# Performance work log

Hardware: AMD Instinct MI355X
Metric: run time of the kernel (lower is better)

Reference implementation:

```python
import jax, jax.numpy as jnp
import numpy as np
import math

B, S, D, H, DFF = 2, 2048, 1024, 16, 4096
DK = D // H
EPS = 1e-6


def setup_inputs() -> dict:
    key = jax.random.key(0)
    ks = jax.random.split(key, 12)
    s = 0.02
    return {
        "x": jax.random.normal(ks[0], (B, S, D), jnp.float32),
        "mask": jnp.ones((B, S), jnp.int32),
        "wq": jax.random.normal(ks[1], (D, D), jnp.float32) * s,
        "bq": jnp.zeros((D,), jnp.float32),
        "wk": jax.random.normal(ks[2], (D, D), jnp.float32) * s,
        "bk": jnp.zeros((D,), jnp.float32),
        "wv": jax.random.normal(ks[3], (D, D), jnp.float32) * s,
        "bv": jnp.zeros((D,), jnp.float32),
        "wo": jax.random.normal(ks[4], (D, D), jnp.float32) * s,
        "bo": jnp.zeros((D,), jnp.float32),
        "g1": jnp.ones((D,), jnp.float32),
        "b1": jnp.zeros((D,), jnp.float32),
        "g2": jnp.ones((D,), jnp.float32),
        "b2": jnp.zeros((D,), jnp.float32),
        "w1": jax.random.normal(ks[5], (DFF, D), jnp.float32) * s,
        "bf1": jnp.zeros((DFF,), jnp.float32),
        "w2": jax.random.normal(ks[6], (D, DFF), jnp.float32) * s,
        "bf2": jnp.zeros((D,), jnp.float32),
    }


def _gelu(x):
    # x * 0.5 * (1 + erf(x / sqrt(2))) -- exact erf-based GELU as in source
    return x * 0.5 * (1.0 + jax.lax.erf(x * (1.0 / math.sqrt(2.0))))


def _layernorm(x, gamma, beta):
    # torch.std uses unbiased (ddof=1); eps is OUTSIDE the sqrt in the source
    mean = jnp.mean(x, axis=-1, keepdims=True)
    std = jnp.std(x, axis=-1, keepdims=True, ddof=1)
    return gamma * (x - mean) / (std + EPS) + beta


def _block(x, mask, wq, bq, wk, bk, wv, bv, wo, bo, g1, b1, g2, b2, w1, bf1, w2, bf2):
    # multi-head attention (dropout is identity in eval mode)
    q = (x @ wq.T + bq).reshape(B, S, H, DK).transpose(0, 2, 1, 3)  # bhsd
    k = (x @ wk.T + bk).reshape(B, S, H, DK).transpose(0, 2, 1, 3)
    v = (x @ wv.T + bv).reshape(B, S, H, DK).transpose(0, 2, 1, 3)
    scores = jnp.einsum("bhsd,bhtd->bhst", q, k) / math.sqrt(DK)
    scores = jnp.where(mask[:, None, None, :] == 0, -1e9, scores)
    attn = jax.nn.softmax(scores, axis=-1)
    cv = jnp.einsum("bhst,bhtd->bhsd", attn, v)
    cv = cv.transpose(0, 2, 1, 3).reshape(B, S, D)
    hd = cv @ wo.T + bo
    # residual + norm1
    hd = _layernorm(x + hd, g1, b1)
    # position-wise FFN with erf GELU
    ff = _gelu(hd @ w1.T + bf1) @ w2.T + bf2
    return _layernorm(hd + ff, g2, b2)


def reference(x, mask, wq, bq, wk, bk, wv, bv, wo, bo, g1, b1, g2, b2, w1, bf1, w2, bf2):
    return _block(x, mask, wq, bq, wk, bk, wv, bv, wo, bo, g1, b1, g2, b2, w1, bf1, w2, bf2)
```

## Files before the change

### kernel.cpp

```cpp
#include <hip/hip_runtime.h>
#include <hip/hip_bf16.h>

#define B_   2
#define S_   2048
#define D_   1024
#define H_   16
#define DK_  64
#define DFF_ 4096
#define M_   (B_*S_)

typedef unsigned short u16;
typedef __attribute__((ext_vector_type(8))) short short8;
typedef __attribute__((ext_vector_type(4))) short bf16x4;
typedef __attribute__((ext_vector_type(4))) float floatx4;

__device__ __forceinline__ u16 f2bf(float f) {
    union { float f; unsigned u; } v; v.f = f;
    unsigned r = v.u + 0x7fffu + ((v.u >> 16) & 1u);
    return (u16)(r >> 16);
}
__device__ __forceinline__ u16 f2bf_fast(float f) {
    __hip_bfloat16 h = __float2bfloat16(f);
    return *reinterpret_cast<u16*>(&h);
}

__device__ __forceinline__ void g2l16(const u16* g, u16* l) {
    __builtin_amdgcn_global_load_lds((const __attribute__((address_space(1))) void*)g,
                                     (__attribute__((address_space(3))) void*)l,
                                     16, 0, 0);
}

__device__ __forceinline__ unsigned lds_off(const void* p) {
    return (unsigned)(unsigned long long)p;
}

#define TRB16(dst, va, IMM)                                                    \
    asm volatile("ds_read_b64_tr_b16 %0, %1 offset:" #IMM                      \
                 : "=v"(dst) : "v"(va))

__global__ __launch_bounds__(256) void cvt_all(
    const float* __restrict__ x,  const float* __restrict__ wq,
    const float* __restrict__ wk, const float* __restrict__ wv,
    const float* __restrict__ wo, const float* __restrict__ w1,
    const float* __restrict__ w2,
    u16* __restrict__ xb, u16* __restrict__ wqkvb, u16* __restrict__ wob,
    u16* __restrict__ w1b, u16* __restrict__ w2b) {
    for (int i = blockIdx.x * 256 + threadIdx.x; i < 4194304;
         i += gridDim.x * 256) {
        const float* s; u16* d; int off;
        if (i < 1048576)      { s = x;  d = xb;    off = i; }
        else if (i < 1310720) { s = wq; d = wqkvb; off = i - 1048576; }
        else if (i < 1572864) { s = wk; d = wqkvb + 1048576; off = i - 1310720; }
        else if (i < 1835008) { s = wv; d = wqkvb + 2097152; off = i - 1572864; }
        else if (i < 2097152) { s = wo; d = wob;   off = i - 1835008; }
        else if (i < 3145728) { s = w1; d = w1b;   off = i - 2097152; }
        else                  { s = w2; d = w2b;   off = i - 3145728; }
        float4 v = reinterpret_cast<const float4*>(s)[off];
        ushort4 o;
        o.x = f2bf(v.x); o.y = f2bf(v.y); o.z = f2bf(v.z); o.w = f2bf(v.w);
        reinterpret_cast<ushort4*>(d)[off] = o;
    }
}

__global__ __launch_bounds__(256) void prep_misc(const float* __restrict__ bq,
                                                 const float* __restrict__ bk,
                                                 const float* __restrict__ bv,
                                                 const int* __restrict__ mask,
                                                 float* __restrict__ bqkv,
                                                 float* __restrict__ mbias) {
    int i = blockIdx.x * 256 + threadIdx.x;
    if (i < 3 * D_) {
        float v = (i < D_) ? bq[i] : (i < 2 * D_) ? bk[i - D_] : bv[i - 2 * D_];
        bqkv[i] = v;
    } else if (i < 3 * D_ + B_ * S_) {
        int k = i - 3 * D_;
        mbias[k] = (mask[k] == 0) ? -1e9f : 0.0f;
    }
}

template <int EPI>
__global__ __launch_bounds__(512, 2) void gemm256_bt(const u16* __restrict__ A,
                                                     const u16* __restrict__ Bw,
                                                     const float* __restrict__ bias,
                                                     u16* __restrict__ Cb,
                                                     int N, int K) {
    __shared__ alignas(16) u16 sA[2][2][8192];
    __shared__ alignas(16) u16 sB[2][2][8192];
    const int tid = threadIdx.x;
    const int wid = tid >> 6, lane = tid & 63;
    const int lrow = lane & 15, lgrp = lane >> 4;
    const int wm = wid >> 2, wn = wid & 3;

    const int nbx = gridDim.x;
    const int nwg = nbx * gridDim.y;
    const int orig = blockIdx.y * nbx + blockIdx.x;
    const int qd = nwg >> 3, rr = nwg & 7, xc = orig & 7, oi = orig >> 3;
    const int swz = (xc < rr ? xc * (qd + 1) : rr * (qd + 1) + (xc - rr) * qd) + oi;
    const int m0 = (swz % nbx) * 256, n0 = (swz / nbx) * 256;

    const u16* Ab = A + (size_t)m0 * K;
    const u16* Bb = Bw + (size_t)n0 * K;
    const int T = K >> 6;

    const int c0 = (wid * 2 + 0) * 64 + lane;
    const int c1 = (wid * 2 + 1) * 64 + lane;
    const int r0 = c0 >> 3, g0 = c0 & 7;
    const int r1 = c1 >> 3, g1 = c1 & 7;
    const size_t so0 = (size_t)r0 * K + (size_t)((g0 ^ (r0 & 7)) * 8);
    const size_t so1 = (size_t)r1 * K + (size_t)((g1 ^ (r1 & 7)) * 8);
    const int d0 = (wid * 2 + 0) * 512;
    const int d1 = (wid * 2 + 1) * 512;

    auto stageA = [&](int par, int half, int kt) {
        const u16* src = Ab + (size_t)(half * 128) * K + kt * 64;
        g2l16(src + so0, &sA[par][half][d0]);
        g2l16(src + so1, &sA[par][half][d1]);
    };
    auto stageB = [&](int par, int half, int kt) {
        const u16* src = Bb + (size_t)(half * 128) * K + kt * 64;
        g2l16(src + so0, &sB[par][half][d0]);
        g2l16(src + so1, &sB[par][half][d1]);
    };

    stageA(0, 0, 0); stageA(0, 1, 0);
    stageB(0, 0, 0); stageB(0, 1, 0);
    if (T > 1) { stageB(1, 0, 1); stageB(1, 1, 1); }
    asm volatile("s_waitcnt vmcnt(4)" ::: "memory");
    asm volatile("s_barrier" ::: "memory");

    floatx4 acc[8][4] = {};
    const int rbase = (wn & 1) * 64;
    const int bhalf = wn >> 1;

    for (int t = 0; t < T; t++) {
        const int par = t & 1;
        const char* baseA = (const char*)&sA[par][wm][0];
        const char* baseB = (const char*)&sB[par][bhalf][0];
        short8 bfr[4][2];
#pragma unroll
        for (int ph = 0; ph < 4; ph++) {
            if (ph == 0) {
#pragma unroll
                for (int nj = 0; nj < 4; nj++) {
                    int rb = rbase + nj * 16 + lrow;
#pragma unroll
                    for (int kk = 0; kk < 2; kk++) {
                        int off = rb * 128 + (((kk * 4 + lgrp) ^ (lrow & 7)) * 16);
                        bfr[nj][kk] = *reinterpret_cast<const short8*>(baseB + off);
                    }
                }
            }
            short8 af[2][2];
#pragma unroll
            for (int a = 0; a < 2; a++) {
                int ra = (2 * ph + a) * 16 + lrow;
#pragma unroll
                for (int kk = 0; kk < 2; kk++) {
                    int off = ra * 128 + (((kk * 4 + lgrp) ^ (lrow & 7)) * 16);
                    af[a][kk] = *reinterpret_cast<const short8*>(baseA + off);
                }
            }
            if (ph == 0) { if (t + 1 < T) stageA(par ^ 1, 0, t + 1); }
            if (ph == 1) { if (t + 1 < T) stageA(par ^ 1, 1, t + 1); }
            if (ph == 2) { if (t + 2 < T) stageB(par, 0, t + 2); }
            if (ph == 3) { if (t + 2 < T) stageB(par, 1, t + 2); }

            asm volatile("s_barrier" ::: "memory");
            asm volatile("s_waitcnt lgkmcnt(0)" ::: "memory");
            __builtin_amdgcn_sched_barrier(0);

            __builtin_amdgcn_s_setprio(1);
#pragma unroll
            for (int a = 0; a < 2; a++)
#pragma unroll
                for (int nj = 0; nj < 4; nj++) {
                    acc[2 * ph + a][nj] = __builtin_amdgcn_mfma_f32_16x16x32_bf16(
                        af[a][0], bfr[nj][0], acc[2 * ph + a][nj], 0, 0, 0);
                    acc[2 * ph + a][nj] = __builtin_amdgcn_mfma_f32_16x16x32_bf16(
                        af[a][1], bfr[nj][1], acc[2 * ph + a][nj], 0, 0, 0);
                }
            __builtin_amdgcn_s_setprio(0);

            if (ph == 3) {
                if (t >= T - 3) asm volatile("s_waitcnt vmcnt(0)" ::: "memory");
                else            asm volatile("s_waitcnt vmcnt(4)" ::: "memory");
            }
            asm volatile("s_barrier" ::: "memory");
        }
    }

#pragma unroll
    for (int mi = 0; mi < 8; mi++) {
        int row = m0 + wm * 128 + mi * 16 + lgrp * 4;
#pragma unroll
        for (int nj = 0; nj < 4; nj++) {
            int col = n0 + wn * 64 + nj * 16 + lrow;
            float bc = bias[col];
#pragma unroll
            for (int j = 0; j < 4; j++) {
                float v = acc[mi][nj][j] + bc;
                if (EPI == 2) v = 0.5f * v * (1.0f + erff(v * 0.70710678118654752f));
                Cb[(size_t)(row + j) * N + col] = f2bf(v);
            }
        }
    }
}

template <int EPI>
__global__ __launch_bounds__(256) void gemm_bt(const u16* __restrict__ A,
                                               const u16* __restrict__ Bw,
                                               const float* __restrict__ bias,
                                               float* __restrict__ Cf,
                                               u16* __restrict__ Cb,
                                               int N, int K) {
    __shared__ u16 sA[128 * 32];
    __shared__ u16 sB[128 * 32];
    const int tid = threadIdx.x;
    const int wid = tid >> 6, lane = tid & 63;
    const int lrow = lane & 15, lgrp = lane >> 4;

    const int nbx = gridDim.x;
    const int nwg = nbx * gridDim.y;
    const int orig = blockIdx.y * nbx + blockIdx.x;
    const int qd = nwg >> 3, rr = nwg & 7, xc = orig & 7, oi = orig >> 3;
    const int swz = (xc < rr ? xc * (qd + 1) : rr * (qd + 1) + (xc - rr) * qd) + oi;
    const int m0 = (swz % nbx) * 128, n0 = (swz / nbx) * 128;

    const int wm = wid >> 1, wn = wid & 1;
    const int ar = lane >> 2, ac = lane & 3;

    floatx4 acc[4][4] = {};
    const u16* Ab = A + (size_t)m0 * K;
    const u16* Bb = Bw + (size_t)n0 * K;

    for (int k0 = 0; k0 < K; k0 += 32) {
#pragma unroll
        for (int i = 0; i < 2; i++) {
            int seg = wid * 2 + i;
            int row = seg * 16 + ar;
            g2l16(Ab + (size_t)row * K + k0 + ac * 8, &sA[seg * 512]);
            g2l16(Bb + (size_t)row * K + k0 + ac * 8, &sB[seg * 512]);
        }
        __syncthreads();
        short8 af[4], bfr[4];
#pragma unroll
        for (int mi = 0; mi < 4; mi++)
            af[mi] = *reinterpret_cast<const short8*>(
                &sA[(wm * 64 + mi * 16 + lrow) * 32 + lgrp * 8]);
#pragma unroll
        for (int ni = 0; ni < 4; ni++)
            bfr[ni] = *reinterpret_cast<const short8*>(
                &sB[(wn * 64 + ni * 16 + lrow) * 32 + lgrp * 8]);
#pragma unroll
        for (int mi = 0; mi < 4; mi++)
#pragma unroll
            for (int ni = 0; ni < 4; ni++)
                acc[mi][ni] = __builtin_amdgcn_mfma_f32_16x16x32_bf16(
                    af[mi], bfr[ni], acc[mi][ni], 0, 0, 0);
        __syncthreads();
    }

#pragma unroll
    for (int mi = 0; mi < 4; mi++) {
        int row = m0 + wm * 64 + mi * 16 + lgrp * 4;
#pragma unroll
        for (int ni = 0; ni < 4; ni++) {
            int col = n0 + wn * 64 + ni * 16 + lrow;
            float bc = bias[col];
#pragma unroll
            for (int j = 0; j < 4; j++) {
                float v = acc[mi][ni][j] + bc;
                if (EPI == 1)
                    Cf[(size_t)(row + j) * N + col] = v;
                else
                    Cb[(size_t)(row + j) * N + col] = f2bf(v);
            }
        }
    }
}

__global__ __launch_bounds__(256) void attn_kernel(const u16* __restrict__ QKV,
                                                   const float* __restrict__ mbias,
                                                   u16* __restrict__ O) {
    const int SD = 3 * D_;
    __shared__ alignas(16) u16 ktL[2][4096];
    __shared__ alignas(16) u16 vtL[2][4096];
    __shared__ alignas(16) u16 pL[4][1024];

    const int orig = blockIdx.y * gridDim.x + blockIdx.x;
    const int swz = (orig & 7) * 128 + (orig >> 3);
    const int qt = swz & 31, bh = swz >> 5;
    const int b = bh >> 4, h = bh & 15;

    const int tid = threadIdx.x, wid = tid >> 6, lane = tid & 63;
    const int lrow = lane & 15, lgrp = lane >> 4;

    const u16* Qp = QKV + h * DK_;
    const u16* Kp = QKV + D_ + h * DK_;
    const u16* Vp = QKV + 2 * D_ + h * DK_;
    const float* mbrow = mbias + b * S_;

    const int qr = qt * 64 + wid * 16 + lrow;
    const u16* qrow = Qp + (size_t)(b * S_ + qr) * SD;
    short8 aq0 = *reinterpret_cast<const short8*>(qrow + lgrp * 8);
    short8 aq1 = *reinterpret_cast<const short8*>(qrow + 32 + lgrp * 8);

    const u16* kq[2];
    const u16* vq[2];
#pragma unroll
    for (int i = 0; i < 2; i++) {
        int s = wid * 2 + i;
        int q8 = s * 64 + lane;
        int krow = q8 >> 3, kcb = q8 & 7;
        kq[i] = Kp + (size_t)(b * S_ + krow) * SD + ((kcb ^ (krow & 7)) * 8);
        int o = s * 512 + lane * 8;
        int vk = ((o >> 6) & 7) * 8 + ((o >> 9) & 1) * 4 + ((o >> 4) & 3);
        int vd = (o >> 10) * 16 + (o & 8);
        vq[i] = Vp + (size_t)(b * S_ + vk) * SD + vd;
    }

    auto issue = [&](int bufIdx) {
        u16* kb_ = ktL[bufIdx];
        u16* vb_ = vtL[bufIdx];
#pragma unroll
        for (int i = 0; i < 2; i++) {
            int s = wid * 2 + i;
            g2l16(kq[i], kb_ + s * 512);
            g2l16(vq[i], vb_ + s * 512);
            kq[i] += 64 * SD;
            vq[i] += 64 * SD;
        }
    };

    floatx4 accO[4] = {};
    float mrun = -1e30f, lrun = 0.f;

    issue(0);
    int cur = 0;
    for (int t = 0; t < S_ / 64; t++) {
        const int kv0 = t * 64;
        if (t < S_ / 64 - 1) {
            issue(cur ^ 1);
            asm volatile("s_waitcnt vmcnt(4)" ::: "memory");
        } else {
            asm volatile("s_waitcnt vmcnt(0)" ::: "memory");
        }
        __builtin_amdgcn_s_barrier();
        asm volatile("" ::: "memory");

        const u16* ktc = ktL[cur];
        const unsigned vva = lds_off(vtL[cur]) + lane * 8;

        float4 mb[4];
#pragma unroll
        for (int ni = 0; ni < 4; ni++)
            mb[ni] = *reinterpret_cast<const float4*>(mbrow + kv0 + ni * 16 + lgrp * 4);

        floatx4 st[4];
        __builtin_amdgcn_s_setprio(1);
#pragma unroll
        for (int ni = 0; ni < 4; ni++) {
            int row = ni * 16 + lrow;
            int off0 = (row * 128 + lgrp * 16) ^ ((lrow & 7) << 4);
            int off1 = (row * 128 + 64 + lgrp * 16) ^ ((lrow & 7) << 4);
            short8 bk0 = *reinterpret_cast<const short8*>((const char*)ktc + off0);
            short8 bk1 = *reinterpret_cast<const short8*>((const char*)ktc + off1);
            floatx4 z = {0.f, 0.f, 0.f, 0.f};
            z = __builtin_amdgcn_mfma_f32_16x16x32_bf16(bk0, aq0, z, 0, 0, 0);
            z = __builtin_amdgcn_mfma_f32_16x16x32_bf16(bk1, aq1, z, 0, 0, 0);
            st[ni] = z;
        }
        __builtin_amdgcn_s_setprio(0);

        float pm[4][4];
#pragma unroll
        for (int ni = 0; ni < 4; ni++) {
            const float* mbp = reinterpret_cast<const float*>(&mb[ni]);
#pragma unroll
            for (int j = 0; j < 4; j++)
                pm[ni][j] = fmaf(st[ni][j], 0.125f, mbp[j]);
        }
        float pmax = pm[0][0];
#pragma unroll
        for (int ni = 0; ni < 4; ni++)
#pragma unroll
            for (int j = 0; j < 4; j++) pmax = fmaxf(pmax, pm[ni][j]);
        pmax = fmaxf(pmax, __shfl_xor(pmax, 16, 64));
        pmax = fmaxf(pmax, __shfl_xor(pmax, 32, 64));

        bool upd = !__all(pmax - mrun <= 8.0f);
        float fac = 1.0f;
        if (upd) {
            float mn = fmaxf(mrun, pmax);
            fac = __expf(mrun - mn);
            mrun = mn;
        }

        float p[4][4];
        float s = 0.f;
#pragma unroll
        for (int ni = 0; ni < 4; ni++)
#pragma unroll
            for (int j = 0; j < 4; j++) {
                float e = __expf(pm[ni][j] - mrun);
                p[ni][j] = e;
                s += e;
            }
        s += __shfl_xor(s, 16, 64);
        s += __shfl_xor(s, 32, 64);
        lrun = lrun * fac + s;

#pragma unroll
        for (int ni = 0; ni < 4; ni++) {
            bf16x4 pw;
#pragma unroll
            for (int j = 0; j < 4; j++) pw[j] = (short)f2bf_fast(p[ni][j]);
            unsigned woff = (unsigned)((lrow * 128 + ni * 32 + lgrp * 8) ^ ((lrow & 7) << 4));
            *reinterpret_cast<bf16x4*>((char*)pL[wid] + woff) = pw;
        }

        if (upd) {
            float f0 = __shfl(fac, lgrp * 4 + 0, 64);
            float f1 = __shfl(fac, lgrp * 4 + 1, 64);
            float f2 = __shfl(fac, lgrp * 4 + 2, 64);
            float f3 = __shfl(fac, lgrp * 4 + 3, 64);
#pragma unroll
            for (int nd = 0; nd < 4; nd++) {
                floatx4 tt = accO[nd];
                tt[0] *= f0; tt[1] *= f1; tt[2] *= f2; tt[3] *= f3;
                accO[nd] = tt;
            }
        }

        asm volatile("s_waitcnt lgkmcnt(0)" ::: "memory");
        __builtin_amdgcn_sched_barrier(0);

        unsigned ra0 = (unsigned)((lrow * 128 + lgrp * 16) ^ ((lrow & 7) << 4));
        unsigned ra1 = (unsigned)((lrow * 128 + 64 + lgrp * 16) ^ ((lrow & 7) << 4));
        short8 ap0 = *reinterpret_cast<const short8*>((const char*)pL[wid] + ra0);
        short8 ap1 = *reinterpret_cast<const short8*>((const char*)pL[wid] + ra1);

        short8 bv0[4], bv1[4];
#pragma unroll
        for (int nd = 0; nd < 4; nd++) {
            unsigned a = vva + nd * 2048;
            bf16x4 t0, t1, t2, t3;
            TRB16(t0, a, 0);
            TRB16(t1, a, 1024);
            TRB16(t2, a, 512);
            TRB16(t3, a, 1536);
            bv0[nd] = __builtin_shufflevector(t0, t1, 0, 1, 2, 3, 4, 5, 6, 7);
            bv1[nd] = __builtin_shufflevector(t2, t3, 0, 1, 2, 3, 4, 5, 6, 7);
        }
        asm volatile("s_waitcnt lgkmcnt(0)" ::: "memory");
        __builtin_amdgcn_sched_barrier(0);

        __builtin_amdgcn_s_setprio(1);
#pragma unroll
        for (int nd = 0; nd < 4; nd++) {
            accO[nd] = __builtin_amdgcn_mfma_f32_16x16x32_bf16(ap0, bv0[nd], accO[nd], 0, 0, 0);
            accO[nd] = __builtin_amdgcn_mfma_f32_16x16x32_bf16(ap1, bv1[nd], accO[nd], 0, 0, 0);
        }
        __builtin_amdgcn_s_setprio(0);

        asm volatile("" ::: "memory");
        __builtin_amdgcn_s_barrier();
        cur ^= 1;
    }

    float linv = 1.0f / lrun;
    float li[4];
#pragma unroll
    for (int j = 0; j < 4; j++) li[j] = __shfl(linv, lgrp * 4 + j, 64);
#pragma unroll
    for (int nd = 0; nd < 4; nd++)
#pragma unroll
        for (int j = 0; j < 4; j++) {
            int r = lgrp * 4 + j;
            float v = accO[nd][j] * li[j];
            O[(size_t)(b * S_ + qt * 64 + wid * 16 + r) * D_ + h * DK_ + nd * 16 + lrow] =
                f2bf_fast(v);
        }
}

__global__ __launch_bounds__(256) void ln_kernel(const float* __restrict__ X,
                                                 const float* __restrict__ R,
                                                 const float* __restrict__ gam,
                                                 const float* __restrict__ bet,
                                                 float* __restrict__ outf,
                                                 u16* __restrict__ outb) {
    __shared__ float ws1[4], ws2[4];
    const int row = blockIdx.x, tid = threadIdx.x;
    const float4 x = reinterpret_cast<const float4*>(X + (size_t)row * D_)[tid];
    const float4 r = reinterpret_cast<const float4*>(R + (size_t)row * D_)[tid];
    float4 v; v.x = x.x + r.x; v.y = x.y + r.y; v.z = x.z + r.z; v.w = x.w + r.w;

    float s = v.x + v.y + v.z + v.w;
#pragma unroll
    for (int m = 32; m >= 1; m >>= 1) s += __shfl_xor(s, m, 64);
    if ((tid & 63) == 0) ws1[tid >> 6] = s;
    __syncthreads();
    float mean = (ws1[0] + ws1[1] + ws1[2] + ws1[3]) * (1.f / D_);

    float4 d; d.x = v.x - mean; d.y = v.y - mean; d.z = v.z - mean; d.w = v.w - mean;
    float q = d.x * d.x + d.y * d.y + d.z * d.z + d.w * d.w;
#pragma unroll
    for (int m = 32; m >= 1; m >>= 1) q += __shfl_xor(q, m, 64);
    if ((tid & 63) == 0) ws2[tid >> 6] = q;
    __syncthreads();
    float var = (ws2[0] + ws2[1] + ws2[2] + ws2[3]) * (1.f / (D_ - 1));
    float inv = 1.f / (sqrtf(var) + 1e-6f);

    const float4 g = reinterpret_cast<const float4*>(gam)[tid];
    const float4 bb = reinterpret_cast<const float4*>(bet)[tid];
    float4 o;
    o.x = g.x * d.x * inv + bb.x;
    o.y = g.y * d.y * inv + bb.y;
    o.z = g.z * d.z * inv + bb.z;
    o.w = g.w * d.w * inv + bb.w;
    if (outf) reinterpret_cast<float4*>(outf + (size_t)row * D_)[tid] = o;
    if (outb) {
        ushort4 ob;
        ob.x = f2bf(o.x); ob.y = f2bf(o.y); ob.z = f2bf(o.z); ob.w = f2bf(o.w);
        reinterpret_cast<ushort4*>(outb + (size_t)row * D_)[tid] = ob;
    }
}

extern "C" void kernel_launch(void* const* d_in, const int* in_sizes, int n_in,
                              void* d_out, int out_size, void* d_ws, size_t ws_size,
                              hipStream_t stream) {
    const float* x    = (const float*)d_in[0];
    const int*   mask = (const int*)d_in[1];
    const float* wq   = (const float*)d_in[2];
    const float* bq   = (const float*)d_in[3];
    const float* wk   = (const float*)d_in[4];
    const float* bk   = (const float*)d_in[5];
    const float* wv   = (const float*)d_in[6];
    const float* bv   = (const float*)d_in[7];
    const float* wo   = (const float*)d_in[8];
    const float* bo   = (const float*)d_in[9];
    const float* g1   = (const float*)d_in[10];
    const float* b1   = (const float*)d_in[11];
    const float* g2   = (const float*)d_in[12];
    const float* b2   = (const float*)d_in[13];
    const float* w1   = (const float*)d_in[14];
    const float* bf1  = (const float*)d_in[15];
    const float* w2   = (const float*)d_in[16];
    const float* bf2  = (const float*)d_in[17];
    float* out = (float*)d_out;

    char* ws = (char*)d_ws;
    size_t off = 0;
    auto alloc = [&](size_t bytes) -> void* {
        void* p = ws + off;
        off += (bytes + 255) & ~(size_t)255;
        return p;
    };
    u16*   xb    = (u16*)  alloc((size_t)M_ * D_ * 2);
    u16*   wqkvb = (u16*)  alloc((size_t)3 * D_ * D_ * 2);
    u16*   wob   = (u16*)  alloc((size_t)D_ * D_ * 2);
    u16*   w1b   = (u16*)  alloc((size_t)DFF_ * D_ * 2);
    u16*   w2b   = (u16*)  alloc((size_t)D_ * DFF_ * 2);
    float* bqkv  = (float*)alloc((size_t)3 * D_ * 4);
    float* mbias = (float*)alloc((size_t)B_ * S_ * 4);
    u16*   qkvb  = (u16*)  alloc((size_t)M_ * 3 * D_ * 2);
    u16*   cvb   = (u16*)  alloc((size_t)M_ * D_ * 2);
    float* projf = (float*)alloc((size_t)M_ * D_ * 4);
    float* hdf   = (float*)alloc((size_t)M_ * D_ * 4);
    u16*   hdb   = (u16*)  alloc((size_t)M_ * D_ * 2);
    u16*   ff1b  = (u16*)  alloc((size_t)M_ * DFF_ * 2);
    float* ff2f  = (float*)alloc((size_t)M_ * D_ * 4);

    cvt_all<<<2048, 256, 0, stream>>>(x, wq, wk, wv, wo, w1, w2,
                                      xb, wqkvb, wob, w1b, w2b);
    prep_misc<<<28, 256, 0, stream>>>(bq, bk, bv, mask, bqkv, mbias);

    gemm256_bt<0><<<dim3(M_ / 256, 3 * D_ / 256), 512, 0, stream>>>(
        xb, wqkvb, bqkv, qkvb, 3 * D_, D_);

    attn_kernel<<<dim3(S_ / 64, B_ * H_), 256, 0, stream>>>(qkvb, mbias, cvb);

    gemm_bt<1><<<dim3(M_ / 128, D_ / 128), 256, 0, stream>>>(
        cvb, wob, bo, projf, nullptr, D_, D_);

    ln_kernel<<<M_, 256, 0, stream>>>(x, projf, g1, b1, hdf, hdb);

    gemm256_bt<2><<<dim3(M_ / 256, DFF_ / 256), 512, 0, stream>>>(
        hdb, w1b, bf1, ff1b, DFF_, D_);

    gemm_bt<1><<<dim3(M_ / 128, D_ / 128), 256, 0, stream>>>(
        ff1b, w2b, bf2, ff2f, nullptr, D_, DFF_);

    ln_kernel<<<M_, 256, 0, stream>>>(hdf, ff2f, g2, b2, out, nullptr);
}
```

Baseline: 455.7 us.

## Widen attention blocks to 128 queries, use exp2 softmax, prefetch V reads early

The attention kernel now runs 8 waves per block over 128 query rows, so each K/V tile loaded into LDS is shared by twice as many queries and each wave issues one async load per tile instead of two. The softmax scale and mask bias are pre-multiplied by log2(e) so the exponentials use the hardware exp2 directly, and the lazy-rescale threshold is scaled to match. The transposed V LDS reads are issued before the softmax math so their latency overlaps with it. The cost is half as many blocks (fewer in flight) and higher register pressure from holding the V fragments across the softmax.

```diff
diff --git a/kernel.cpp b/kernel.cpp
--- a/kernel.cpp
+++ b/kernel.cpp
@@ -22,6 +22,10 @@
 __device__ __forceinline__ u16 f2bf_fast(float f) {
     __hip_bfloat16 h = __float2bfloat16(f);
     return *reinterpret_cast<u16*>(&h);
+}
+
+__device__ __forceinline__ float exp2_fast(float f) {
+    return __builtin_amdgcn_exp2f(f);
 }
 
 __device__ __forceinline__ void g2l16(const u16* g, u16* l) {
@@ -74,7 +78,7 @@
         bqkv[i] = v;
     } else if (i < 3 * D_ + B_ * S_) {
         int k = i - 3 * D_;
-        mbias[k] = (mask[k] == 0) ? -1e9f : 0.0f;
+        mbias[k] = (mask[k] == 0) ? -1.44269504e9f : 0.0f;
     }
 }
 
@@ -279,17 +283,17 @@
     }
 }
 
-__global__ __launch_bounds__(256) void attn_kernel(const u16* __restrict__ QKV,
+__global__ __launch_bounds__(512) void attn_kernel(const u16* __restrict__ QKV,
                                                    const float* __restrict__ mbias,
                                                    u16* __restrict__ O) {
     const int SD = 3 * D_;
     __shared__ alignas(16) u16 ktL[2][4096];
     __shared__ alignas(16) u16 vtL[2][4096];
-    __shared__ alignas(16) u16 pL[4][1024];
+    __shared__ alignas(16) u16 pL[8][1024];
 
     const int orig = blockIdx.y * gridDim.x + blockIdx.x;
-    const int swz = (orig & 7) * 128 + (orig >> 3);
-    const int qt = swz & 31, bh = swz >> 5;
+    const int swz = (orig & 7) * 64 + (orig >> 3);
+    const int qt = swz & 15, bh = swz >> 4;
     const int b = bh >> 4, h = bh & 15;
 
     const int tid = threadIdx.x, wid = tid >> 6, lane = tid & 63;
@@ -300,40 +304,29 @@
     const u16* Vp = QKV + 2 * D_ + h * DK_;
     const float* mbrow = mbias + b * S_;
 
-    const int qr = qt * 64 + wid * 16 + lrow;
+    const int qr = qt * 128 + wid * 16 + lrow;
     const u16* qrow = Qp + (size_t)(b * S_ + qr) * SD;
     short8 aq0 = *reinterpret_cast<const short8*>(qrow + lgrp * 8);
     short8 aq1 = *reinterpret_cast<const short8*>(qrow + 32 + lgrp * 8);
 
-    const u16* kq[2];
-    const u16* vq[2];
-#pragma unroll
-    for (int i = 0; i < 2; i++) {
-        int s = wid * 2 + i;
-        int q8 = s * 64 + lane;
-        int krow = q8 >> 3, kcb = q8 & 7;
-        kq[i] = Kp + (size_t)(b * S_ + krow) * SD + ((kcb ^ (krow & 7)) * 8);
-        int o = s * 512 + lane * 8;
-        int vk = ((o >> 6) & 7) * 8 + ((o >> 9) & 1) * 4 + ((o >> 4) & 3);
-        int vd = (o >> 10) * 16 + (o & 8);
-        vq[i] = Vp + (size_t)(b * S_ + vk) * SD + vd;
-    }
+    const int q8 = wid * 64 + lane;
+    const int krow = q8 >> 3, kcb = q8 & 7;
+    const u16* kq = Kp + (size_t)(b * S_ + krow) * SD + ((kcb ^ (krow & 7)) * 8);
+    const int ov = wid * 512 + lane * 8;
+    const int vk = ((ov >> 6) & 7) * 8 + ((ov >> 9) & 1) * 4 + ((ov >> 4) & 3);
+    const int vd = (ov >> 10) * 16 + (ov & 8);
+    const u16* vq = Vp + (size_t)(b * S_ + vk) * SD + vd;
 
     auto issue = [&](int bufIdx) {
-        u16* kb_ = ktL[bufIdx];
-        u16* vb_ = vtL[bufIdx];
-#pragma unroll
-        for (int i = 0; i < 2; i++) {
-            int s = wid * 2 + i;
-            g2l16(kq[i], kb_ + s * 512);
-            g2l16(vq[i], vb_ + s * 512);
-            kq[i] += 64 * SD;
-            vq[i] += 64 * SD;
-        }
+        g2l16(kq, &ktL[bufIdx][wid * 512]);
+        g2l16(vq, &vtL[bufIdx][wid * 512]);
+        kq += 64 * SD;
+        vq += 64 * SD;
     };
 
     floatx4 accO[4] = {};
     float mrun = -1e30f, lrun = 0.f;
+    const float SC2 = 0.18033688011112042f;
 
     issue(0);
     int cur = 0;
@@ -341,7 +334,7 @@
         const int kv0 = t * 64;
         if (t < S_ / 64 - 1) {
             issue(cur ^ 1);
-            asm volatile("s_waitcnt vmcnt(4)" ::: "memory");
+            asm volatile("s_waitcnt vmcnt(2)" ::: "memory");
         } else {
             asm volatile("s_waitcnt vmcnt(0)" ::: "memory");
         }
@@ -372,13 +365,23 @@
         }
         __builtin_amdgcn_s_setprio(0);
 
+        bf16x4 vt0[4], vt1[4], vt2[4], vt3[4];
+#pragma unroll
+        for (int nd = 0; nd < 4; nd++) {
+            unsigned a = vva + nd * 2048;
+            TRB16(vt0[nd], a, 0);
+            TRB16(vt1[nd], a, 1024);
+            TRB16(vt2[nd], a, 512);
+            TRB16(vt3[nd], a, 1536);
+        }
+
         float pm[4][4];
 #pragma unroll
         for (int ni = 0; ni < 4; ni++) {
             const float* mbp = reinterpret_cast<const float*>(&mb[ni]);
 #pragma unroll
             for (int j = 0; j < 4; j++)
-                pm[ni][j] = fmaf(st[ni][j], 0.125f, mbp[j]);
+                pm[ni][j] = fmaf(st[ni][j], SC2, mbp[j]);
         }
         float pmax = pm[0][0];
 #pragma unroll
@@ -388,11 +391,11 @@
         pmax = fmaxf(pmax, __shfl_xor(pmax, 16, 64));
         pmax = fmaxf(pmax, __shfl_xor(pmax, 32, 64));
 
-        bool upd = !__all(pmax - mrun <= 8.0f);
+        bool upd = !__all(pmax - mrun <= 11.5f);
         float fac = 1.0f;
         if (upd) {
             float mn = fmaxf(mrun, pmax);
-            fac = __expf(mrun - mn);
+            fac = exp2_fast(mrun - mn);
             mrun = mn;
         }
 
@@ -402,7 +405,7 @@
         for (int ni = 0; ni < 4; ni++)
 #pragma unroll
             for (int j = 0; j < 4; j++) {
-                float e = __expf(pm[ni][j] - mrun);
+                float e = exp2_fast(pm[ni][j] - mrun);
                 p[ni][j] = e;
                 s += e;
             }
@@ -440,26 +443,13 @@
         short8 ap0 = *reinterpret_cast<const short8*>((const char*)pL[wid] + ra0);
         short8 ap1 = *reinterpret_cast<const short8*>((const char*)pL[wid] + ra1);
 
-        short8 bv0[4], bv1[4];
+        __builtin_amdgcn_s_setprio(1);
 #pragma unroll
         for (int nd = 0; nd < 4; nd++) {
-            unsigned a = vva + nd * 2048;
-            bf16x4 t0, t1, t2, t3;
-            TRB16(t0, a, 0);
-            TRB16(t1, a, 1024);
-            TRB16(t2, a, 512);
-            TRB16(t3, a, 1536);
-            bv0[nd] = __builtin_shufflevector(t0, t1, 0, 1, 2, 3, 4, 5, 6, 7);
-            bv1[nd] = __builtin_shufflevector(t2, t3, 0, 1, 2, 3, 4, 5, 6, 7);
-        }
-        asm volatile("s_waitcnt lgkmcnt(0)" ::: "memory");
-        __builtin_amdgcn_sched_barrier(0);
-
-        __builtin_amdgcn_s_setprio(1);
-#pragma unroll
-        for (int nd = 0; nd < 4; nd++) {
-            accO[nd] = __builtin_amdgcn_mfma_f32_16x16x32_bf16(ap0, bv0[nd], accO[nd], 0, 0, 0);
-            accO[nd] = __builtin_amdgcn_mfma_f32_16x16x32_bf16(ap1, bv1[nd], accO[nd], 0, 0, 0);
+            short8 bv0 = __builtin_shufflevector(vt0[nd], vt1[nd], 0, 1, 2, 3, 4, 5, 6, 7);
+            short8 bv1 = __builtin_shufflevector(vt2[nd], vt3[nd], 0, 1, 2, 3, 4, 5, 6, 7);
+            accO[nd] = __builtin_amdgcn_mfma_f32_16x16x32_bf16(ap0, bv0, accO[nd], 0, 0, 0);
+            accO[nd] = __builtin_amdgcn_mfma_f32_16x16x32_bf16(ap1, bv1, accO[nd], 0, 0, 0);
         }
         __builtin_amdgcn_s_setprio(0);
 
@@ -478,7 +468,7 @@
         for (int j = 0; j < 4; j++) {
             int r = lgrp * 4 + j;
             float v = accO[nd][j] * li[j];
-            O[(size_t)(b * S_ + qt * 64 + wid * 16 + r) * D_ + h * DK_ + nd * 16 + lrow] =
+            O[(size_t)(b * S_ + qt * 128 + wid * 16 + r) * D_ + h * DK_ + nd * 16 + lrow] =
                 f2bf_fast(v);
         }
 }
@@ -578,7 +568,7 @@
     gemm256_bt<0><<<dim3(M_ / 256, 3 * D_ / 256), 512, 0, stream>>>(
         xb, wqkvb, bqkv, qkvb, 3 * D_, D_);
 
-    attn_kernel<<<dim3(S_ / 64, B_ * H_), 256, 0, stream>>>(qkvb, mbias, cvb);
+    attn_kernel<<<dim3(S_ / 128, B_ * H_), 512, 0, stream>>>(qkvb, mbias, cvb);
 
     gemm_bt<1><<<dim3(M_ / 128, D_ / 128), 256, 0, stream>>>(
         cvb, wob, bo, projf, nullptr, D_, D_);
```

New measurement: 424.4 us. 1.07x faster.
